# Performance work log

Measured on AMD Instinct MI355X. Metric: run time of the kernel, lower is better.

## Reference

```python
import jax, jax.numpy as jnp
import numpy as np

B, T, C = 2, 2048, 2048
H, HKV = 32, 8
D = C // H            # head_dim = 64
G = H // HKV          # groups = 4
ROPE_BASE = 10000.0


def _rotate_half(x):
    x1, x2 = jnp.split(x, 2, axis=-1)
    return jnp.concatenate((-x2, x1), axis=-1)


def _rope_tables(seq_len, dim):
    inv_freq = 1.0 / (ROPE_BASE ** (jnp.arange(0, dim, 2, dtype=jnp.float32) / dim))
    t = jnp.arange(seq_len, dtype=jnp.float32)
    freqs = jnp.outer(t, inv_freq)          # [T, D/2]
    emb = jnp.concatenate((freqs, freqs), axis=-1)  # [T, D]
    return jnp.cos(emb), jnp.sin(emb)


def setup_inputs() -> dict:
    key = jax.random.key(0)
    ks = jax.random.split(key, 5)
    s = 0.02
    return {
        "x": jax.random.normal(ks[0], (B, T, C), jnp.float32),
        "Wq": jax.random.normal(ks[1], (C, C), jnp.float32) * s,
        "Wk": jax.random.normal(ks[2], (HKV * D, C), jnp.float32) * s,
        "Wv": jax.random.normal(ks[3], (HKV * D, C), jnp.float32) * s,
        "Wo": jax.random.normal(ks[4], (C, C), jnp.float32) * s,
    }


def reference(x, Wq, Wk, Wv, Wo):
    b, t, c = x.shape
    # fused QKV projections (nn.Linear: y = x @ W.T)
    q = (x @ Wq.T).reshape(b, t, H, D).transpose(0, 2, 1, 3)      # [B,H,T,D]
    k = (x @ Wk.T).reshape(b, t, HKV, D).transpose(0, 2, 1, 3)    # [B,HKV,T,D]
    v = (x @ Wv.T).reshape(b, t, HKV, D).transpose(0, 2, 1, 3)

    # RoPE (start_pos = 0)
    cos, sin = _rope_tables(t, D)           # [T, D] each
    cos = cos[None, None]                   # [1,1,T,D]
    sin = sin[None, None]
    q = q * cos + _rotate_half(q) * sin
    k = k * cos + _rotate_half(k) * sin

    # GQA head expansion (repeat_interleave on head dim)
    k = jnp.repeat(k, G, axis=1)            # [B,H,T,D]
    v = jnp.repeat(v, G, axis=1)

    # causal attention
    scale = 1.0 / jnp.sqrt(jnp.asarray(D, jnp.float32))
    scores = jnp.einsum('bhqd,bhkd->bhqk', q, k) * scale          # [B,H,T,T]
    causal = jnp.tril(jnp.ones((t, t), dtype=bool))
    scores = jnp.where(causal[None, None], scores, -jnp.inf)
    attn = jax.nn.softmax(scores.astype(jnp.float32), axis=-1).astype(q.dtype)
    out = jnp.einsum('bhqk,bhkd->bhqd', attn, v)                  # [B,H,T,D]
    out = out.transpose(0, 2, 1, 3).reshape(b, t, c)
    return out @ Wo.T
```

## Files before the change

### kernel.cpp

```cpp
#include <hip/hip_runtime.h>
#include <hip/hip_bf16.h>
#include <math.h>

typedef short short8 __attribute__((ext_vector_type(8)));
typedef float floatx4 __attribute__((ext_vector_type(4)));

typedef __attribute__((address_space(1))) unsigned int as1_u32;
typedef __attribute__((address_space(3))) unsigned int as3_u32;

__device__ __forceinline__ void load_lds16(const void* g, void* l) {
  __builtin_amdgcn_global_load_lds((const as1_u32*)g, (as3_u32*)l, 16, 0, 0);
}

__device__ __forceinline__ unsigned short f2bf(float f) {
  __bf16 h = (__bf16)f;
  return __builtin_bit_cast(unsigned short, h);
}

#define TB 2
#define TT 2048
#define TC 2048
#define QKN 2560
#define KOFF 2048
#define SCALE_Q 0.18033688f

__global__ __launch_bounds__(256) void cast_all(
    const float* __restrict__ x, const float* __restrict__ wq,
    const float* __restrict__ wk, const float* __restrict__ wv,
    const float* __restrict__ wo,
    unsigned short* __restrict__ xb, unsigned short* __restrict__ wqkv,
    unsigned short* __restrict__ wob, float2* __restrict__ ropeTab) {
  if (blockIdx.x < 256) {
    const int idx = blockIdx.x * 256 + threadIdx.x;
    const int t = idx >> 5, d = idx & 31;
    const float inv = exp2f((float)d * -0.4152410119f);
    float sn, cs;
    sincosf((float)t * inv, &sn, &cs);
    ropeTab[idx] = make_float2(cs, sn);
  }
  long i4 = (long)blockIdx.x * 256 + threadIdx.x;
  const float* src;
  unsigned short* dst;
  if (i4 < 2097152)      { src = x;  dst = xb; }
  else if (i4 < 3145728) { src = wq; dst = wqkv;           i4 -= 2097152; }
  else if (i4 < 3407872) { src = wk; dst = wqkv + 4194304; i4 -= 3145728; }
  else if (i4 < 3670016) { src = wv; dst = wqkv + 5242880; i4 -= 3407872; }
  else                   { src = wo; dst = wob;            i4 -= 3670016; }
  float4 v = ((const float4*)src)[i4];
  ushort4 o;
  o.x = f2bf(v.x); o.y = f2bf(v.y); o.z = f2bf(v.z); o.w = f2bf(v.w);
  ((ushort4*)dst)[i4] = o;
}

__global__ __launch_bounds__(256) void gemm_qkv(const unsigned short* __restrict__ A,
                                                const unsigned short* __restrict__ Bw,
                                                unsigned short* __restrict__ qk,
                                                unsigned short* __restrict__ vT,
                                                const float2* __restrict__ ropeTab) {
  __shared__ unsigned short As[128 * 64];
  __shared__ unsigned short Bs[128 * 64];
  const int K = 2048;
  const int tid = threadIdx.x;
  const int lane = tid & 63, w = tid >> 6;
  const int quad = lane >> 4, l15 = lane & 15;
  const int wm = w >> 1, wn = w & 1;
  const int lin = blockIdx.y * 24 + blockIdx.x;
  const int sub = lin >> 3;
  const int m0 = (sub / 3) * 128;
  const int n0 = ((lin & 7) * 3 + sub % 3) * 128;

  floatx4 acc[4][4];
#pragma unroll
  for (int i = 0; i < 4; ++i)
#pragma unroll
    for (int j = 0; j < 4; ++j) acc[i][j] = (floatx4){0.f, 0.f, 0.f, 0.f};

  const int ar = tid >> 3;
  const int ac = (((tid & 7) ^ (ar & 7)) * 8);
  const unsigned short* Abase = A + (size_t)(m0 + ar) * K + ac;
  const unsigned short* Bbase = Bw + (size_t)(n0 + ar) * K + ac;

  for (int k0 = 0; k0 < K; k0 += 64) {
    __syncthreads();
#pragma unroll
    for (int p = 0; p < 4; ++p) {
      load_lds16(Abase + (size_t)(p * 32) * K + k0, (char*)As + p * 4096 + tid * 16);
      load_lds16(Bbase + (size_t)(p * 32) * K + k0, (char*)Bs + p * 4096 + tid * 16);
    }
    __syncthreads();
#pragma unroll
    for (int ks = 0; ks < 2; ++ks) {
      short8 af[4], bfr[4];
      const int key = (((ks << 2) + quad) ^ (l15 & 7)) << 4;
#pragma unroll
      for (int i = 0; i < 4; ++i)
        af[i] = *(const short8*)((const char*)As + (wm * 64 + i * 16 + l15) * 128 + key);
#pragma unroll
      for (int j = 0; j < 4; ++j)
        bfr[j] = *(const short8*)((const char*)Bs + (wn * 64 + j * 16 + l15) * 128 + key);
#pragma unroll
      for (int i = 0; i < 4; ++i)
#pragma unroll
        for (int j = 0; j < 4; ++j)
          acc[i][j] = __builtin_amdgcn_mfma_f32_16x16x32_bf16(af[i], bfr[j], acc[i][j], 0, 0, 0);
    }
  }

  const int colb = n0 + wn * 64;
  if (colb < QKN) {
    const float qscale = (colb < KOFF) ? SCALE_Q : 1.0f;
#pragma unroll
    for (int i = 0; i < 4; ++i) {
      const int rowb = m0 + wm * 64 + i * 16 + quad * 4;
      const int tb = rowb & (TT - 1);
#pragma unroll
      for (int j = 0; j < 2; ++j) {
        const int col = colb + j * 16 + l15;
        const int d = j * 16 + l15;
#pragma unroll
        for (int r = 0; r < 4; ++r) {
          const float2 cssn = ropeTab[(tb + r) * 32 + d];
          const float a = acc[i][j][r], b2 = acc[i][j + 2][r];
          const float qa = (a * cssn.x - b2 * cssn.y) * qscale;
          const float qb = (b2 * cssn.x + a * cssn.y) * qscale;
          unsigned short* p = qk + (size_t)(rowb + r) * QKN + col;
          p[0] = f2bf(qa);
          p[32] = f2bf(qb);
        }
      }
    }
  } else {
#pragma unroll
    for (int i = 0; i < 4; ++i) {
      const int rowb = m0 + wm * 64 + i * 16 + quad * 4;
#pragma unroll
      for (int j = 0; j < 4; ++j) {
        const int col = colb + j * 16 + l15;
        ushort4 pk;
        pk.x = f2bf(acc[i][j][0]); pk.y = f2bf(acc[i][j][1]);
        pk.z = f2bf(acc[i][j][2]); pk.w = f2bf(acc[i][j][3]);
        *(ushort4*)(vT + (size_t)(col - 2560) * 4096 + rowb) = pk;
      }
    }
  }
}

__global__ __launch_bounds__(256) void gemm_nt_f32(const unsigned short* __restrict__ A,
                                                   const unsigned short* __restrict__ Bw,
                                                   float* __restrict__ C,
                                                   int M, int N, int K) {
  __shared__ unsigned short As[128 * 64];
  __shared__ unsigned short Bs[128 * 64];
  const int tid = threadIdx.x;
  const int lane = tid & 63, w = tid >> 6;
  const int quad = lane >> 4, l15 = lane & 15;
  const int wm = w >> 1, wn = w & 1;
  const int lin = blockIdx.y * 16 + blockIdx.x;
  const int sub = lin >> 3;
  const int m0 = (sub >> 1) * 128;
  const int n0 = ((lin & 7) * 2 + (sub & 1)) * 128;

  floatx4 acc[4][4];
#pragma unroll
  for (int i = 0; i < 4; ++i)
#pragma unroll
    for (int j = 0; j < 4; ++j) acc[i][j] = (floatx4){0.f, 0.f, 0.f, 0.f};

  const int ar = tid >> 3;
  const int ac = (((tid & 7) ^ (ar & 7)) * 8);
  const unsigned short* Abase = A + (size_t)(m0 + ar) * K + ac;
  const unsigned short* Bbase = Bw + (size_t)(n0 + ar) * K + ac;

  for (int k0 = 0; k0 < K; k0 += 64) {
    __syncthreads();
#pragma unroll
    for (int p = 0; p < 4; ++p) {
      load_lds16(Abase + (size_t)(p * 32) * K + k0, (char*)As + p * 4096 + tid * 16);
      load_lds16(Bbase + (size_t)(p * 32) * K + k0, (char*)Bs + p * 4096 + tid * 16);
    }
    __syncthreads();
#pragma unroll
    for (int ks = 0; ks < 2; ++ks) {
      short8 af[4], bfr[4];
      const int key = (((ks << 2) + quad) ^ (l15 & 7)) << 4;
#pragma unroll
      for (int i = 0; i < 4; ++i)
        af[i] = *(const short8*)((const char*)As + (wm * 64 + i * 16 + l15) * 128 + key);
#pragma unroll
      for (int j = 0; j < 4; ++j)
        bfr[j] = *(const short8*)((const char*)Bs + (wn * 64 + j * 16 + l15) * 128 + key);
#pragma unroll
      for (int i = 0; i < 4; ++i)
#pragma unroll
        for (int j = 0; j < 4; ++j)
          acc[i][j] = __builtin_amdgcn_mfma_f32_16x16x32_bf16(af[i], bfr[j], acc[i][j], 0, 0, 0);
    }
  }
#pragma unroll
  for (int i = 0; i < 4; ++i) {
    const int row = m0 + wm * 64 + i * 16 + quad * 4;
#pragma unroll
    for (int j = 0; j < 4; ++j) {
      const int col = n0 + wn * 64 + j * 16 + l15;
#pragma unroll
      for (int r = 0; r < 4; ++r)
        C[(size_t)(row + r) * N + col] = acc[i][j][r];
    }
  }
}

#define LDSA_K(buf) (lds + (buf) * 8192)
#define LDSA_V(buf) (lds + 16384 + (buf) * 8192)
#define LDSA_P      (lds + 32768)

__global__ __launch_bounds__(256) void attn_kernel(const unsigned short* __restrict__ qk,
                                                   const unsigned short* __restrict__ vT,
                                                   unsigned short* __restrict__ attn) {
  const int hcode = blockIdx.x;
  const int h = (hcode & 7) * 4 + (hcode >> 3);
  const int bx = blockIdx.y;
  const int b = blockIdx.z;
  const int hk = h >> 2;
  const int tid = threadIdx.x;
  const int w = tid >> 6, lane = tid & 63, quad = lane >> 4, l15 = lane & 15;

  __shared__ char lds[51200];
  unsigned short* Pq = (unsigned short*)(LDSA_P + w * 4608);

  const int srow = tid >> 3;
  const int sgrp = ((tid & 7) ^ (srow & 7));

  const short8 ones = {16256, 16256, 16256, 16256, 16256, 16256, 16256, 16256};

  for (int pass = 0; pass < 2; ++pass) {
    const int qt = pass ? (15 - bx) : bx;
    const size_t rowQ = (size_t)(b * TT + qt * 128);

    {
      const unsigned short* qsrc = qk + (rowQ + srow) * QKN + h * 64 + sgrp * 8;
#pragma unroll
      for (int p = 0; p < 4; ++p)
        load_lds16(qsrc + (size_t)p * 32 * QKN, lds + p * 4096 + tid * 16);
    }
    __syncthreads();
    short8 qf[2][2];
#pragma unroll
    for (int i = 0; i < 2; ++i)
#pragma unroll
      for (int ks = 0; ks < 2; ++ks)
        qf[i][ks] = *(const short8*)(lds + (w * 32 + i * 16 + l15) * 128 +
                                     ((((ks << 2) + quad) ^ (l15 & 7)) << 4));
    __syncthreads();

    floatx4 accO[2][4], accL[2];
#pragma unroll
    for (int i = 0; i < 2; ++i) {
      accL[i] = (floatx4){0.f, 0.f, 0.f, 0.f};
#pragma unroll
      for (int j = 0; j < 4; ++j) accO[i][j] = (floatx4){0.f, 0.f, 0.f, 0.f};
    }

    {
      const unsigned short* ksrc =
          qk + (size_t)(b * TT + srow) * QKN + KOFF + hk * 64 + sgrp * 8;
      load_lds16(ksrc, LDSA_K(0) + tid * 16);
      load_lds16(ksrc + (size_t)32 * QKN, LDSA_K(0) + 4096 + tid * 16);
      const unsigned short* vsrc =
          vT + (size_t)(hk * 64 + srow) * 4096 + b * TT + sgrp * 8;
      load_lds16(vsrc, LDSA_V(0) + tid * 16);
      load_lds16(vsrc + (size_t)32 * 4096, LDSA_V(0) + 4096 + tid * 16);
    }
    __syncthreads();

    const int ktmax = 2 * qt + 1;
    for (int kt = 0; kt <= ktmax; ++kt) {
      const int cur = kt & 1, nxt = cur ^ 1;
      if (kt < ktmax) {
        const unsigned short* ksrc =
            qk + (size_t)(b * TT + (kt + 1) * 64 + srow) * QKN + KOFF + hk * 64 + sgrp * 8;
        load_lds16(ksrc, LDSA_K(nxt) + tid * 16);
        load_lds16(ksrc + (size_t)32 * QKN, LDSA_K(nxt) + 4096 + tid * 16);
        const unsigned short* vsrc =
            vT + (size_t)(hk * 64 + srow) * 4096 + b * TT + (kt + 1) * 64 + sgrp * 8;
        load_lds16(vsrc, LDSA_V(nxt) + tid * 16);
        load_lds16(vsrc + (size_t)32 * 4096, LDSA_V(nxt) + 4096 + tid * 16);
      }

      const char* Ks = LDSA_K(cur);
      floatx4 st[2][4];
#pragma unroll
      for (int jm = 0; jm < 4; ++jm) {
        const int krow = jm * 16 + l15;
        const short8 kf0 = *(const short8*)(Ks + krow * 128 + ((quad ^ (l15 & 7)) << 4));
        const short8 kf1 = *(const short8*)(Ks + krow * 128 + (((4 + quad) ^ (l15 & 7)) << 4));
#pragma unroll
        for (int i = 0; i < 2; ++i) {
          floatx4 z = (floatx4){0.f, 0.f, 0.f, 0.f};
          z = __builtin_amdgcn_mfma_f32_16x16x32_bf16(kf0, qf[i][0], z, 0, 0, 0);
          st[i][jm] = __builtin_amdgcn_mfma_f32_16x16x32_bf16(kf1, qf[i][1], z, 0, 0, 0);
        }
      }

      const bool domask = (kt >= 2 * qt);
#pragma unroll
      for (int i = 0; i < 2; ++i) {
        const int qg = qt * 128 + w * 32 + i * 16 + l15;
#pragma unroll
        for (int jm = 0; jm < 4; ++jm) {
          float e0 = exp2f(st[i][jm][0]);
          float e1 = exp2f(st[i][jm][1]);
          float e2 = exp2f(st[i][jm][2]);
          float e3 = exp2f(st[i][jm][3]);
          if (domask) {
            const int kg = kt * 64 + jm * 16 + quad * 4;
            if (kg > qg) e0 = 0.f;
            if (kg + 1 > qg) e1 = 0.f;
            if (kg + 2 > qg) e2 = 0.f;
            if (kg + 3 > qg) e3 = 0.f;
          }
          ushort4 pk;
          pk.x = f2bf(e0); pk.y = f2bf(e1); pk.z = f2bf(e2); pk.w = f2bf(e3);
          *(ushort4*)(Pq + (i * 16 + l15) * 72 + jm * 16 + quad * 4) = pk;
        }
      }
      asm volatile("s_waitcnt lgkmcnt(0)" ::: "memory");

      const char* Vt = LDSA_V(cur);
#pragma unroll
      for (int ks = 0; ks < 2; ++ks) {
        short8 pf[2];
#pragma unroll
        for (int i2 = 0; i2 < 2; ++i2)
          pf[i2] = *(const short8*)(Pq + (i2 * 16 + l15) * 72 + ks * 32 + quad * 8);
        accL[0] = __builtin_amdgcn_mfma_f32_16x16x32_bf16(pf[0], ones, accL[0], 0, 0, 0);
        accL[1] = __builtin_amdgcn_mfma_f32_16x16x32_bf16(pf[1], ones, accL[1], 0, 0, 0);
#pragma unroll
        for (int jd = 0; jd < 4; ++jd) {
          const int d = jd * 16 + l15;
          const short8 vf = *(const short8*)(Vt + d * 128 +
                                             ((((ks << 2) + quad) ^ (l15 & 7)) << 4));
          accO[0][jd] = __builtin_amdgcn_mfma_f32_16x16x32_bf16(pf[0], vf, accO[0][jd], 0, 0, 0);
          accO[1][jd] = __builtin_amdgcn_mfma_f32_16x16x32_bf16(pf[1], vf, accO[1][jd], 0, 0, 0);
        }
      }
      __syncthreads();
    }

#pragma unroll
    for (int i2 = 0; i2 < 2; ++i2) {
#pragma unroll
      for (int jd = 0; jd < 4; ++jd) {
        const int col = h * 64 + jd * 16 + l15;
#pragma unroll
        for (int r = 0; r < 4; ++r) {
          const size_t row = rowQ + w * 32 + i2 * 16 + quad * 4 + r;
          attn[row * TC + col] = f2bf(accO[i2][jd][r] / accL[i2][r]);
        }
      }
    }
  }
}

extern "C" void kernel_launch(void* const* d_in, const int* in_sizes, int n_in,
                              void* d_out, int out_size, void* d_ws, size_t ws_size,
                              hipStream_t stream) {
  const float* x = (const float*)d_in[0];
  const float* Wq = (const float*)d_in[1];
  const float* Wk = (const float*)d_in[2];
  const float* Wv = (const float*)d_in[3];
  const float* Wo = (const float*)d_in[4];
  float* out = (float*)d_out;

  char* ws = (char*)d_ws;
  unsigned short* xb   = (unsigned short*)(ws);
  unsigned short* wqkv = (unsigned short*)(ws + 16777216);
  unsigned short* wob  = (unsigned short*)(ws + 29360128);
  unsigned short* qk   = (unsigned short*)(ws + 37748736);
  unsigned short* vT   = (unsigned short*)(ws + 58720256);
  unsigned short* attn = (unsigned short*)(ws + 62914560);
  float2* ropeTab = (float2*)(ws + 62914560);

  cast_all<<<18432, 256, 0, stream>>>(x, Wq, Wk, Wv, Wo, xb, wqkv, wob, ropeTab);
  gemm_qkv<<<dim3(24, 32), 256, 0, stream>>>(xb, wqkv, qk, vT, ropeTab);
  attn_kernel<<<dim3(32, 8, 2), 256, 0, stream>>>(qk, vT, attn);
  gemm_nt_f32<<<dim3(16, 32), 256, 0, stream>>>(attn, wob, out, 4096, TC, 2048);
}
```

Before: 297.9 us.

## Unroll attention KV loop by two with static buffers and hoisted V loads

Unrolls the attention K/V tile loop in pairs through a lambda, so the double-buffer index, prefetch predicate and causal-mask offset become compile-time constants. Masking now runs only on the last two diagonal tiles. V fragments are loaded from LDS before the softmax exponentials so their latency can overlap with the math. The grid is also reordered so query tiles are the fastest-varying block index, replacing the earlier head swizzle. This changes which blocks share K/V in cache, and the hoisted V fragments add register pressure.

```diff
diff --git a/kernel.cpp b/kernel.cpp
--- a/kernel.cpp
+++ b/kernel.cpp
@@ -209,26 +209,21 @@
   }
 }
 
-#define LDSA_K(buf) (lds + (buf) * 8192)
-#define LDSA_V(buf) (lds + 16384 + (buf) * 8192)
-#define LDSA_P      (lds + 32768)
-
 __global__ __launch_bounds__(256) void attn_kernel(const unsigned short* __restrict__ qk,
                                                    const unsigned short* __restrict__ vT,
                                                    unsigned short* __restrict__ attn) {
-  const int hcode = blockIdx.x;
-  const int h = (hcode & 7) * 4 + (hcode >> 3);
-  const int bx = blockIdx.y;
-  const int b = blockIdx.z;
+  const int bx = blockIdx.x;
+  const int h = blockIdx.y, b = blockIdx.z;
   const int hk = h >> 2;
   const int tid = threadIdx.x;
   const int w = tid >> 6, lane = tid & 63, quad = lane >> 4, l15 = lane & 15;
 
   __shared__ char lds[51200];
-  unsigned short* Pq = (unsigned short*)(LDSA_P + w * 4608);
+  unsigned short* Pq = (unsigned short*)(lds + 32768 + w * 4608);
 
   const int srow = tid >> 3;
   const int sgrp = ((tid & 7) ^ (srow & 7));
+  const int relbase = w * 32 + l15;
 
   const short8 ones = {16256, 16256, 16256, 16256, 16256, 16256, 16256, 16256};
 
@@ -260,33 +255,32 @@
       for (int j = 0; j < 4; ++j) accO[i][j] = (floatx4){0.f, 0.f, 0.f, 0.f};
     }
 
-    {
-      const unsigned short* ksrc =
-          qk + (size_t)(b * TT + srow) * QKN + KOFF + hk * 64 + sgrp * 8;
-      load_lds16(ksrc, LDSA_K(0) + tid * 16);
-      load_lds16(ksrc + (size_t)32 * QKN, LDSA_K(0) + 4096 + tid * 16);
-      const unsigned short* vsrc =
-          vT + (size_t)(hk * 64 + srow) * 4096 + b * TT + sgrp * 8;
-      load_lds16(vsrc, LDSA_V(0) + tid * 16);
-      load_lds16(vsrc + (size_t)32 * 4096, LDSA_V(0) + 4096 + tid * 16);
-    }
-    __syncthreads();
-
-    const int ktmax = 2 * qt + 1;
-    for (int kt = 0; kt <= ktmax; ++kt) {
-      const int cur = kt & 1, nxt = cur ^ 1;
-      if (kt < ktmax) {
-        const unsigned short* ksrc =
-            qk + (size_t)(b * TT + (kt + 1) * 64 + srow) * QKN + KOFF + hk * 64 + sgrp * 8;
-        load_lds16(ksrc, LDSA_K(nxt) + tid * 16);
-        load_lds16(ksrc + (size_t)32 * QKN, LDSA_K(nxt) + 4096 + tid * 16);
-        const unsigned short* vsrc =
-            vT + (size_t)(hk * 64 + srow) * 4096 + b * TT + (kt + 1) * 64 + sgrp * 8;
-        load_lds16(vsrc, LDSA_V(nxt) + tid * 16);
-        load_lds16(vsrc + (size_t)32 * 4096, LDSA_V(nxt) + 4096 + tid * 16);
-      }
-
-      const char* Ks = LDSA_K(cur);
+    const unsigned short* kptr =
+        qk + (size_t)(b * TT + srow) * QKN + KOFF + hk * 64 + sgrp * 8;
+    const unsigned short* vptr =
+        vT + (size_t)(hk * 64 + srow) * 4096 + b * TT + sgrp * 8;
+
+    load_lds16(kptr, lds + tid * 16);
+    load_lds16(kptr + (size_t)32 * QKN, lds + 4096 + tid * 16);
+    load_lds16(vptr, lds + 16384 + tid * 16);
+    load_lds16(vptr + (size_t)32 * 4096, lds + 16384 + 4096 + tid * 16);
+    kptr += (size_t)64 * QKN;
+    vptr += 64;
+    __syncthreads();
+
+    auto step = [&](const int BUF, const bool PREF, const int MREL) {
+      if (PREF) {
+        char* kd = lds + ((BUF ^ 1) * 8192);
+        char* vd = lds + 16384 + ((BUF ^ 1) * 8192);
+        load_lds16(kptr, kd + tid * 16);
+        load_lds16(kptr + (size_t)32 * QKN, kd + 4096 + tid * 16);
+        load_lds16(vptr, vd + tid * 16);
+        load_lds16(vptr + (size_t)32 * 4096, vd + 4096 + tid * 16);
+        kptr += (size_t)64 * QKN;
+        vptr += 64;
+      }
+
+      const char* Ks = lds + BUF * 8192;
       floatx4 st[2][4];
 #pragma unroll
       for (int jm = 0; jm < 4; ++jm) {
@@ -301,22 +295,32 @@
         }
       }
 
-      const bool domask = (kt >= 2 * qt);
+      const char* Vt = lds + 16384 + BUF * 8192;
+      short8 vf[2][4];
+#pragma unroll
+      for (int ks = 0; ks < 2; ++ks)
+#pragma unroll
+        for (int jd = 0; jd < 4; ++jd) {
+          const int d = jd * 16 + l15;
+          vf[ks][jd] = *(const short8*)(Vt + d * 128 +
+                                        ((((ks << 2) + quad) ^ (l15 & 7)) << 4));
+        }
+
 #pragma unroll
       for (int i = 0; i < 2; ++i) {
-        const int qg = qt * 128 + w * 32 + i * 16 + l15;
 #pragma unroll
         for (int jm = 0; jm < 4; ++jm) {
           float e0 = exp2f(st[i][jm][0]);
           float e1 = exp2f(st[i][jm][1]);
           float e2 = exp2f(st[i][jm][2]);
           float e3 = exp2f(st[i][jm][3]);
-          if (domask) {
-            const int kg = kt * 64 + jm * 16 + quad * 4;
-            if (kg > qg) e0 = 0.f;
-            if (kg + 1 > qg) e1 = 0.f;
-            if (kg + 2 > qg) e2 = 0.f;
-            if (kg + 3 > qg) e3 = 0.f;
+          if (MREL >= 0) {
+            const int rel = relbase + i * 16 - MREL;
+            const int kg = jm * 16 + quad * 4;
+            if (kg > rel) e0 = 0.f;
+            if (kg + 1 > rel) e1 = 0.f;
+            if (kg + 2 > rel) e2 = 0.f;
+            if (kg + 3 > rel) e3 = 0.f;
           }
           ushort4 pk;
           pk.x = f2bf(e0); pk.y = f2bf(e1); pk.z = f2bf(e2); pk.w = f2bf(e3);
@@ -325,7 +329,6 @@
       }
       asm volatile("s_waitcnt lgkmcnt(0)" ::: "memory");
 
-      const char* Vt = LDSA_V(cur);
 #pragma unroll
       for (int ks = 0; ks < 2; ++ks) {
         short8 pf[2];
@@ -336,15 +339,19 @@
         accL[1] = __builtin_amdgcn_mfma_f32_16x16x32_bf16(pf[1], ones, accL[1], 0, 0, 0);
 #pragma unroll
         for (int jd = 0; jd < 4; ++jd) {
-          const int d = jd * 16 + l15;
-          const short8 vf = *(const short8*)(Vt + d * 128 +
-                                             ((((ks << 2) + quad) ^ (l15 & 7)) << 4));
-          accO[0][jd] = __builtin_amdgcn_mfma_f32_16x16x32_bf16(pf[0], vf, accO[0][jd], 0, 0, 0);
-          accO[1][jd] = __builtin_amdgcn_mfma_f32_16x16x32_bf16(pf[1], vf, accO[1][jd], 0, 0, 0);
+          accO[0][jd] = __builtin_amdgcn_mfma_f32_16x16x32_bf16(pf[0], vf[ks][jd], accO[0][jd], 0, 0, 0);
+          accO[1][jd] = __builtin_amdgcn_mfma_f32_16x16x32_bf16(pf[1], vf[ks][jd], accO[1][jd], 0, 0, 0);
         }
       }
       __syncthreads();
-    }
+    };
+
+    for (int t2 = 0; t2 < qt; ++t2) {
+      step(0, true, -1);
+      step(1, true, -1);
+    }
+    step(0, true, 0);
+    step(1, false, 64);
 
 #pragma unroll
     for (int i2 = 0; i2 < 2; ++i2) {
@@ -382,6 +389,6 @@
 
   cast_all<<<18432, 256, 0, stream>>>(x, Wq, Wk, Wv, Wo, xb, wqkv, wob, ropeTab);
   gemm_qkv<<<dim3(24, 32), 256, 0, stream>>>(xb, wqkv, qk, vT, ropeTab);
-  attn_kernel<<<dim3(32, 8, 2), 256, 0, stream>>>(qk, vT, attn);
+  attn_kernel<<<dim3(8, 32, 2), 256, 0, stream>>>(qk, vT, attn);
   gemm_nt_f32<<<dim3(16, 32), 256, 0, stream>>>(attn, wob, out, 4096, TC, 2048);
 }
```

After: 293.1 us. Within noise of the previous version (-1.6%).
